# Kernel tuning notes

Hardware: AMD Instinct MI355X
Metric: run time of the kernel (lower is better)

Reference implementation:

```python
import jax, jax.numpy as jnp
import numpy as np

# Module hyperparameters (from init_kwargs)
H, E, K = 16, 8, 2          # heads, experts per head, top-k
P, PV = 64, 64              # q/k and v projection sizes
D = 1024                    # state / input / output size
B, T = 8, 512               # batch, sequence length (self-attention)
R = 2 * T - 1               # number of relative offsets


def setup_inputs() -> dict:
    key = jax.random.key(0)
    ks = jax.random.split(key, 9)
    std_in = 1.0 / np.sqrt(D)
    std_out = 1.0 / np.sqrt(H * PV)
    return {
        "x": jax.random.normal(ks[0], (B, T, D), jnp.float32),
        "pe": jax.random.normal(ks[1], (R, D), jnp.float32),
        "w_sel_o": jax.random.normal(ks[2], (H, E, D), jnp.float32) * std_in,
        "w_sel_v": jax.random.normal(ks[3], (H, E, D), jnp.float32) * std_in,
        "W_q": jax.random.normal(ks[4], (H, E, D, P), jnp.float32) * std_in,
        "W_k": jax.random.normal(ks[5], (H, E, D, P), jnp.float32) * std_in,
        "W_v": jax.random.normal(ks[6], (H, E, D, PV), jnp.float32) * std_in,
        "W_o": jax.random.normal(ks[7], (H, E, PV, D), jnp.float32) * std_out,
        "W_pos": jax.random.normal(ks[8], (H * P, D), jnp.float32) * std_in,
    }


def _gates(x, w_sel):
    # sigmoid selection per head, top-K experts kept with their gate values.
    logits = jnp.einsum('btd,hed->bthe', x, w_sel)
    g = jax.nn.sigmoid(logits)
    vals, idx = jax.lax.top_k(g, K)                      # [B,T,H,K]
    onehot = jax.nn.one_hot(idx, E, dtype=g.dtype)        # [B,T,H,K,E]
    return jnp.einsum('bthk,bthke->bthe', vals, onehot)   # sparse dense gates [B,T,H,E]


def _moe_proj(x, W, gates):
    # x [B,T,D], W [H,E,D,P], gates [B,T,H,E] -> [B,T,H,P]
    out = jnp.zeros(x.shape[:2] + (H, W.shape[-1]), x.dtype)
    for e in range(E):  # fixed small expert loop; avoids [B,T,H,E,P] intermediate
        out = out + gates[..., e, None] * jnp.einsum('btd,hdp->bthp', x, W[:, e])
    return out


def reference(x, pe, w_sel_o, w_sel_v, W_q, W_k, W_v, W_o, W_pos):
    # MoEUT selection sharing: q shares o's selection, k shares v's selection.
    g_qo = _gates(x, w_sel_o)
    g_kv = _gates(x, w_sel_v)

    q = _moe_proj(x, W_q, g_qo)   # [B,T,H,P]
    k = _moe_proj(x, W_k, g_kv)   # [B,T,H,P]
    v = _moe_proj(x, W_v, g_kv)   # [B,T,H,PV]

    scale = 1.0 / np.sqrt(P)
    k_pos = (pe @ W_pos.T).reshape(R, H, P)               # relative-position keys

    s_cont = jnp.einsum('bthp,bshp->bhts', q, k)          # content scores
    s_rel = jnp.einsum('bthp,rhp->bhtr', q, k_pos)        # scores over relative offsets
    t_idx = jnp.arange(T)
    rel = t_idx[None, :] - t_idx[:, None] + (T - 1)       # rel index for (t, s)
    s_pos = s_rel[:, :, t_idx[:, None], rel]              # Transformer-XL shift -> [B,H,T,T]

    scores = (s_cont + s_pos) * scale
    causal = t_idx[None, :] <= t_idx[:, None]
    scores = jnp.where(causal[None, None], scores, jnp.asarray(-1e9, scores.dtype))
    attn = jax.nn.softmax(scores, axis=-1)
    ctx = jnp.einsum('bhts,bshv->bthv', attn, v)          # [B,T,H,PV]

    # MoE output projection with o-selection
    out = jnp.zeros((x.shape[0], x.shape[1], W_o.shape[-1]), x.dtype)
    for e in range(E):
        out = out + jnp.einsum('bthv,hvd->btd', ctx * g_qo[..., e, None], W_o[:, e])
    return out
```

## Files before the change

kernel.cpp:

```cpp
#include <hip/hip_runtime.h>
#include <hip/hip_bf16.h>
#include <math.h>

#define H_ 16
#define E_ 8
#define D_ 1024
#define P_ 64
#define PV_ 64
#define B_ 8
#define T_ 512
#define R_ 1023
#define BT_ 4096
#define CAP_ 1024
#define PROWS_ 192
#define PTILES_ 4

typedef __attribute__((ext_vector_type(8))) unsigned short ushort8;
typedef __attribute__((ext_vector_type(4))) unsigned short ushort4v;
typedef __attribute__((ext_vector_type(8))) short short8;
typedef __attribute__((ext_vector_type(4))) float f32x4;

__device__ inline float bf2f(unsigned short u) {
  union { unsigned int i; float f; } c; c.i = ((unsigned int)u) << 16; return c.f;
}
// ... 62 lines not shown
  }
  __syncthreads();

  int wave = tid >> 6, lane = tid & 63;
  const float4* wt4 = (const float4*)wt + (size_t)ks * 256 * 64 + lane;
  float4 acc[8];
#pragma unroll
  for (int r = 0; r < 8; ++r) acc[r] = (float4){0.f, 0.f, 0.f, 0.f};

  for (int k4b = 0; k4b < 64; ++k4b) {
    float4 wv0 = wt4[(size_t)(k4b * 4 + 0) * 64];
    float4 wv1 = wt4[(size_t)(k4b * 4 + 1) * 64];
    float4 wv2 = wt4[(size_t)(k4b * 4 + 2) * 64];
    float4 wv3 = wt4[(size_t)(k4b * 4 + 3) * 64];
#pragma unroll
    for (int r = 0; r < 8; ++r) {
      float4 xv = ((const float4*)xs[wave * 8 + r])[k4b];
      acc[r].x += xv.x * wv0.x + xv.y * wv1.x + xv.z * wv2.x + xv.w * wv3.x;
      acc[r].y += xv.x * wv0.y + xv.y * wv1.y + xv.z * wv2.y + xv.w * wv3.y;
      acc[r].z += xv.x * wv0.z + xv.y * wv1.z + xv.z * wv2.z + xv.w * wv3.z;
      acc[r].w += xv.x * wv0.w + xv.y * wv1.w + xv.z * wv2.w + xv.w * wv3.w;
    }
  }

#pragma unroll
  for (int r = 0; r < 8; ++r)
    *(float4*)&part[((size_t)(bt0 + wave * 8 + r) * 4 + ks) * 256 + lane * 4] =
        acc[r];
}

__global__ __launch_bounds__(256) void gates_combine(
    const float* __restrict__ part, int* __restrict__ cnt,
    int* __restrict__ lidx, float* __restrict__ lg,
    float* __restrict__ coefs) {
  __shared__ float gv[8][2][H_][E_];
  int tid = threadIdx.x;
  int bt0 = blockIdx.x * 8;

  {
    int set = tid >> 7, he = tid & 127;
    int h = he >> 3, e = he & 7;
#pragma unroll
    for (int r = 0; r < 8; ++r) {
      const float* p = &part[(size_t)(bt0 + r) * 4 * 256 + tid];
      float v = ((p[0] + p[256]) + p[512]) + p[768];
      gv[r][set][h][e] = 1.f / (1.f + expf(-v));
    }
  }
  __syncthreads();

  {
    int r = tid >> 5, st = (tid >> 4) & 1, hh = tid & 15;
    int bt = bt0 + r;
    const float* g = gv[r][st][hh];
    int i1 = 0; float v1 = g[0];
    for (int ee = 1; ee < 8; ee++) if (g[ee] > v1) { v1 = g[ee]; i1 = ee; }
    int i2 = (i1 == 0) ? 1 : 0; float v2 = g[i2];
    for (int ee = 0; ee < 8; ee++) {
      if (ee == i1) continue;
      if (g[ee] > v2) { v2 = g[ee]; i2 = ee; }
    }
    int base1 = ((st * H_ + hh) * E_ + i1) * 2 + 0;
    int p1 = atomicAdd(&cnt[base1], 1);
    lidx[(size_t)base1 * CAP_ + p1] = bt;
    lg[(size_t)base1 * CAP_ + p1] = v1;
    int base2 = ((st * H_ + hh) * E_ + i2) * 2 + 1;
    int p2 = atomicAdd(&cnt[base2], 1);
    lidx[(size_t)base2 * CAP_ + p2] = bt;
    lg[(size_t)base2 * CAP_ + p2] = v2;
    if (st == 0) {
#pragma unroll
      for (int ee = 0; ee < 8; ee++) {
        float c = (ee == i1) ? v1 : ((ee == i2) ? v2 : 0.f);
        coefs[((size_t)bt * H_ + hh) * E_ + ee] = c;
      }
    }
  }
}

__global__ __launch_bounds__(256) void proj_q2_mfma(
    const unsigned short* __restrict__ xb, const float* __restrict__ W,
    const int* __restrict__ cnt, const int* __restrict__ lidx,
    const float* __restrict__ lg, unsigned short* __restrict__ out0,
    unsigned short* __restrict__ out1) {
  int he = blockIdx.x, tile = blockIdx.y;
  int base0 = he * 2 + 0, base1 = he * 2 + 1;
  int n0 = cnt[base0], n1 = cnt[base1];
  int start = tile * PROWS_;
  if (start >= n0 && start >= n1) return;
  int m0 = min(PROWS_, max(0, n0 - start));
  int m1 = min(PROWS_, max(0, n1 - start));

  __shared__ int ridx0[PROWS_], ridx1[PROWS_];
  __shared__ float rgs0[PROWS_], rgs1[PROWS_];
  __shared__ __align__(16) unsigned short As0[PROWS_][72];
  __shared__ __align__(16) unsigned short As1[PROWS_][72];
  __shared__ __align__(16) unsigned short Bs[64][72];
  int tid = threadIdx.x;
  for (int i = tid; i < PROWS_; i += 256) {
    int v0i = 0, v1i = 0; float g0 = 0.f, g1 = 0.f;
    if (i < m0) {
      v0i = lidx[(size_t)base0 * CAP_ + start + i];
      g0 = lg[(size_t)base0 * CAP_ + start + i];
    }
    if (i < m1) {
      v1i = lidx[(size_t)base1 * CAP_ + start + i];
      g1 = lg[(size_t)base1 * CAP_ + start + i];
    }
    ridx0[i] = v0i; rgs0[i] = g0;
    ridx1[i] = v1i; rgs1[i] = g1;
  }
  __syncthreads();

  int wave = tid >> 6, lane = tid & 63;
  int lr = lane & 15, lk = (lane >> 4) << 3;
  f32x4 acc0[3][4] = {}, acc1[3][4] = {};
  const float* Wb = W + (size_t)he * D_ * P_;

  int sr = tid >> 2, sseg = (tid & 3) << 4;
  int c4 = (tid & 15) * 4;
  int drb = tid >> 4;

  for (int d0 = 0; d0 < D_; d0 += 64) {
#pragma unroll
    for (int i = 0; i < 3; ++i) {
      int row = i * 64 + sr;
      const unsigned short* x0 = xb + (size_t)ridx0[row] * D_ + d0 + sseg;
      *(ushort8*)&As0[row][sseg] = *(const ushort8*)x0;
      *(ushort8*)&As0[row][sseg + 8] = *(const ushort8*)(x0 + 8);
      const unsigned short* x1 = xb + (size_t)ridx1[row] * D_ + d0 + sseg;
      *(ushort8*)&As1[row][sseg] = *(const ushort8*)x1;
      *(ushort8*)&As1[row][sseg + 8] = *(const ushort8*)(x1 + 8);
    }
#pragma unroll
    for (int pass = 0; pass < 4; ++pass) {
      int dr = pass * 16 + drb;
      float4 wv = *(const float4*)&Wb[(size_t)(d0 + dr) * P_ + c4];
      Bs[c4 + 0][dr] = f2bf(wv.x);
      Bs[c4 + 1][dr] = f2bf(wv.y);
      Bs[c4 + 2][dr] = f2bf(wv.z);
      Bs[c4 + 3][dr] = f2bf(wv.w);
    }
    __syncthreads();
#pragma unroll
    for (int kk = 0; kk < 2; ++kk) {
      short8 af0[3], af1[3], bfr[4];
#pragma unroll
      for (int mm = 0; mm < 3; ++mm) {
        af0[mm] = *(const short8*)&As0[wave * 48 + mm * 16 + lr][kk * 32 + lk];
        af1[mm] = *(const short8*)&As1[wave * 48 + mm * 16 + lr][kk * 32 + lk];
      }
#pragma unroll
      for (int nn = 0; nn < 4; ++nn)
        bfr[nn] = *(const short8*)&Bs[nn * 16 + lr][kk * 32 + lk];
#pragma unroll
      for (int mm = 0; mm < 3; ++mm)
#pragma unroll
        for (int nn = 0; nn < 4; ++nn) {
          acc0[mm][nn] = __builtin_amdgcn_mfma_f32_16x16x32_bf16(
              af0[mm], bfr[nn], acc0[mm][nn], 0, 0, 0);
          acc1[mm][nn] = __builtin_amdgcn_mfma_f32_16x16x32_bf16(
              af1[mm], bfr[nn], acc1[mm][nn], 0, 0, 0);
        }
    }
    __syncthreads();
  }

  int h = he >> 3;
#pragma unroll
  for (int mm = 0; mm < 3; ++mm) {
#pragma unroll
    for (int r = 0; r < 4; ++r) {
      int row = wave * 48 + mm * 16 + (lane >> 4) * 4 + r;
      if (row < m0) {
        int bt = ridx0[row]; float g = rgs0[row];
        int b = bt >> 9, t = bt & 511;
        unsigned short* orow = out0 + ((size_t)((b * H_ + h) * T_) + t) * P_;
#pragma unroll
        for (int nn = 0; nn < 4; ++nn)
          orow[nn * 16 + lr] = f2bf(g * acc0[mm][nn][r]);
      }
      if (row < m1) {
        int bt = ridx1[row]; float g = rgs1[row];
        int b = bt >> 9, t = bt & 511;
        unsigned short* orow = out1 + ((size_t)((b * H_ + h) * T_) + t) * P_;
#pragma unroll
        for (int nn = 0; nn < 4; ++nn)
          orow[nn * 16 + lr] = f2bf(g * acc1[mm][nn][r]);
      }
    }
  }
}

__global__ __launch_bounds__(256) void proj_kv_mfma(
    const unsigned short* __restrict__ xb, const float* __restrict__ Wk,
    const float* __restrict__ Wv, const int* __restrict__ cnt,
    const int* __restrict__ lidx, const float* __restrict__ lg,
    unsigned short* __restrict__ outk, unsigned short* __restrict__ outv,
    int slot) {
  int he = blockIdx.x, tile = blockIdx.y;
  int base = (128 + he) * 2 + slot;
  int n = cnt[base];
  int start = tile * PROWS_;
  if (start >= n) return;
  int m = min(PROWS_, n - start);

  __shared__ int ridx[PROWS_];
  __shared__ float rgs[PROWS_];
  __shared__ __align__(16) unsigned short As[PROWS_][72];
  __shared__ __align__(16) unsigned short Bk[64][72];
  __shared__ __align__(16) unsigned short Bv[64][72];
  int tid = threadIdx.x;
  for (int i = tid; i < PROWS_; i += 256) {
    int vi = 0; float g = 0.f;
    if (i < m) {
      vi = lidx[(size_t)base * CAP_ + start + i];
      g = lg[(size_t)base * CAP_ + start + i];
    }
    ridx[i] = vi; rgs[i] = g;
  }
  __syncthreads();

  int wave = tid >> 6, lane = tid & 63;
  int lr = lane & 15, lk = (lane >> 4) << 3;
  f32x4 acck[3][4] = {}, accv[3][4] = {};
  const float* Wkb = Wk + (size_t)he * D_ * P_;
  const float* Wvb = Wv + (size_t)he * D_ * P_;

  int sr = tid >> 2, sseg = (tid & 3) << 4;
  int c4 = (tid & 15) * 4;
  int drb = tid >> 4;

  for (int d0 = 0; d0 < D_; d0 += 64) {
#pragma unroll
    for (int i = 0; i < 3; ++i) {
      int row = i * 64 + sr;
      const unsigned short* xrow = xb + (size_t)ridx[row] * D_ + d0 + sseg;
      *(ushort8*)&As[row][sseg] = *(const ushort8*)xrow;
      *(ushort8*)&As[row][sseg + 8] = *(const ushort8*)(xrow + 8);
    }
#pragma unroll
    for (int pass = 0; pass < 4; ++pass) {
      int dr = pass * 16 + drb;
      float4 wv = *(const float4*)&Wkb[(size_t)(d0 + dr) * P_ + c4];
      Bk[c4 + 0][dr] = f2bf(wv.x);
      Bk[c4 + 1][dr] = f2bf(wv.y);
      Bk[c4 + 2][dr] = f2bf(wv.z);
      Bk[c4 + 3][dr] = f2bf(wv.w);
      float4 wv2 = *(const float4*)&Wvb[(size_t)(d0 + dr) * P_ + c4];
      Bv[c4 + 0][dr] = f2bf(wv2.x);
      Bv[c4 + 1][dr] = f2bf(wv2.y);
      Bv[c4 + 2][dr] = f2bf(wv2.z);
      Bv[c4 + 3][dr] = f2bf(wv2.w);
    }
    __syncthreads();
#pragma unroll
    for (int kk = 0; kk < 2; ++kk) {
      short8 af[3], b1[4], b2[4];
#pragma unroll
      for (int mm = 0; mm < 3; ++mm)
        af[mm] = *(const short8*)&As[wave * 48 + mm * 16 + lr][kk * 32 + lk];
#pragma unroll
      for (int nn = 0; nn < 4; ++nn) {
        b1[nn] = *(const short8*)&Bk[nn * 16 + lr][kk * 32 + lk];
        b2[nn] = *(const short8*)&Bv[nn * 16 + lr][kk * 32 + lk];
      }
#pragma unroll
      for (int mm = 0; mm < 3; ++mm)
#pragma unroll
        for (int nn = 0; nn < 4; ++nn) {
          acck[mm][nn] = __builtin_amdgcn_mfma_f32_16x16x32_bf16(
              af[mm], b1[nn], acck[mm][nn], 0, 0, 0);
          accv[mm][nn] = __builtin_amdgcn_mfma_f32_16x16x32_bf16(
              af[mm], b2[nn], accv[mm][nn], 0, 0, 0);
        }
    }
    __syncthreads();
  }

  int h = he >> 3;
#pragma unroll
  for (int mm = 0; mm < 3; ++mm) {
#pragma unroll
    for (int r = 0; r < 4; ++r) {
      int row = wave * 48 + mm * 16 + (lane >> 4) * 4 + r;
      if (row < m) {
        int bt = ridx[row]; float g = rgs[row];
        int b = bt >> 9, t = bt & 511;
        size_t off = ((size_t)((b * H_ + h) * T_) + t) * P_;
        unsigned short* okr = outk + off;
        unsigned short* ovr = outv + off;
        if (slot == 0) {
#pragma unroll
          for (int nn = 0; nn < 4; ++nn) {
            okr[nn * 16 + lr] = f2bf(g * acck[mm][nn][r]);
            ovr[nn * 16 + lr] = f2bf(g * accv[mm][nn][r]);
          }
        } else {
#pragma unroll
          for (int nn = 0; nn < 4; ++nn) {
            int c = nn * 16 + lr;
            okr[c] = f2bf(bf2f(okr[c]) + g * acck[mm][nn][r]);
            ovr[c] = f2bf(bf2f(ovr[c]) + g * accv[mm][nn][r]);
          }
        }
      }
    }
  }
}

__global__ __launch_bounds__(256) void cvt_pos_kernel(
    const float* __restrict__ pe, const float* __restrict__ Wp,
    unsigned short* __restrict__ peb, unsigned short* __restrict__ wpb) {
  int bid = blockIdx.x;
  const float* src;
  unsigned short* dst;
  if (bid < R_) { src = pe + (size_t)bid * D_; dst = peb + (size_t)bid * D_; }
  else { src = Wp + (size_t)(bid - R_) * D_; dst = wpb + (size_t)(bid - R_) * D_; }
  int tid = threadIdx.x;
  float4 w = ((const float4*)src)[tid];
  ushort4v o = {f2bf(w.x), f2bf(w.y), f2bf(w.z), f2bf(w.w)};
  *(ushort4v*)&dst[tid * 4] = o;
}

__global__ __launch_bounds__(256) void kpos_mfma(
    const unsigned short* __restrict__ peb, const unsigned short* __restrict__ wpb,
    unsigned short* __restrict__ kposb) {
  __shared__ __align__(16) unsigned short As[64][72];
  __shared__ __align__(16) unsigned short Bs[64][72];
  int tid = threadIdx.x, mt = blockIdx.x, nt = blockIdx.y;
  int wave = tid >> 6, lane = tid & 63;
  int wr = wave >> 1, wc = wave & 1;
  int lrow = lane & 15, lk = (lane >> 4) << 3;
  f32x4 acc[2][2] = {};
  int sr = tid >> 2, sseg = (tid & 3) << 4;

  for (int d0 = 0; d0 < D_; d0 += 64) {
    {
      const unsigned short* arow = &peb[(size_t)(mt * 64 + sr) * D_ + d0 + sseg];
      *(ushort8*)&As[sr][sseg] = *(const ushort8*)arow;
      *(ushort8*)&As[sr][sseg + 8] = *(const ushort8*)(arow + 8);
      const unsigned short* brow = &wpb[(size_t)(nt * 64 + sr) * D_ + d0 + sseg];
      *(ushort8*)&Bs[sr][sseg] = *(const ushort8*)brow;
      *(ushort8*)&Bs[sr][sseg + 8] = *(const ushort8*)(brow + 8);
    }
    __syncthreads();
#pragma unroll
    for (int kk = 0; kk < 2; ++kk) {
      short8 af[2], bfr[2];
#pragma unroll
      for (int mm = 0; mm < 2; ++mm)
        af[mm] = *(const short8*)&As[wr * 32 + mm * 16 + lrow][kk * 32 + lk];
#pragma unroll
      for (int nn = 0; nn < 2; ++nn)
        bfr[nn] = *(const short8*)&Bs[wc * 32 + nn * 16 + lrow][kk * 32 + lk];
#pragma unroll
      for (int mm = 0; mm < 2; ++mm)
#pragma unroll
        for (int nn = 0; nn < 2; ++nn)
          acc[mm][nn] = __builtin_amdgcn_mfma_f32_16x16x32_bf16(
              af[mm], bfr[nn], acc[mm][nn], 0, 0, 0);
    }
    __syncthreads();
  }

  int orow0 = mt * 64 + wr * 32 + (lane >> 4) * 4;
  int ocol0 = nt * 64 + wc * 32 + lrow;
#pragma unroll
  for (int mm = 0; mm < 2; ++mm)
#pragma unroll
    for (int nn = 0; nn < 2; ++nn)
#pragma unroll
      for (int r = 0; r < 4; ++r)
        kposb[(size_t)(orow0 + mm * 16 + r) * 1024 + ocol0 + nn * 16] =
            f2bf(acc[mm][nn][r]);
}

__global__ __launch_bounds__(256) void attn_mfma(
    const unsigned short* __restrict__ q0, const unsigned short* __restrict__ q1,
    const unsigned short* __restrict__ k, const unsigned short* __restrict__ v,
    const unsigned short* __restrict__ kposb, unsigned short* __restrict__ ctx) {
  int b = blockIdx.x, h = blockIdx.y, qt = blockIdx.z;
  int t0 = qt << 6;
  int tid = threadIdx.x, wave = tid >> 6, lane = tid & 63;
  int lr = lane & 15, lkg = lane >> 4;
  int lk = lkg << 3;

  __shared__ __align__(16) unsigned short Ks[64][72];
  __shared__ __align__(16) unsigned short VTs[64][72];
  __shared__ __align__(16) unsigned short Srl[64][136];

  size_t bh = (size_t)(b * H_ + h);
  const unsigned short* kb = k + bh * T_ * 64;
  const unsigned short* vb = v + bh * T_ * 64;

  short8 qf[2];
  {
    size_t qoff = (bh * T_ + (size_t)(t0 + wave * 16 + lr)) * 64;
    const unsigned short* q0r = q0 + qoff;
    const unsigned short* q1r = q1 + qoff;
#pragma unroll
    for (int kk = 0; kk < 2; ++kk) {
      ushort8 a0 = *(const ushort8*)&q0r[kk * 32 + lk];
      ushort8 a1 = *(const ushort8*)&q1r[kk * 32 + lk];
      short8 o;
#pragma unroll
      for (int j = 0; j < 8; ++j)
        o[j] = (short)f2bf(bf2f(a0[j]) + bf2f(a1[j]));
      qf[kk] = o;
    }
  }

  float m_run[4], l_run[4];
  f32x4 oacc[4];
#pragma unroll
  for (int r = 0; r < 4; ++r) { m_run[r] = -1e30f; l_run[r] = 0.f; }
#pragma unroll
  for (int nn = 0; nn < 4; ++nn) oacc[nn] = (f32x4){0.f, 0.f, 0.f, 0.f};

  int row_local = wave * 16 + lkg * 4;
  int krow_s = tid >> 1, kseg_s = (tid & 1) * 32;
  int t2 = tid & 127;
  int vr0 = (t2 & 15) * 4, vcs = (t2 >> 4) * 8;

  for (int st = 0; st <= qt; ++st) {
    int s0 = st << 6;
    if (tid < 128) {
      const unsigned short* krow = kb + (size_t)(s0 + krow_s) * 64 + kseg_s;
#pragma unroll
      for (int i = 0; i < 4; ++i)
        *(ushort8*)&Ks[krow_s][kseg_s + i * 8] = *(const ushort8*)(krow + i * 8);
    } else {
      ushort8 vr[4];
#pragma unroll
      for (int i = 0; i < 4; ++i)
        vr[i] = *(const ushort8*)&vb[(size_t)(s0 + vr0 + i) * 64 + vcs];
#pragma unroll
      for (int j = 0; j < 8; ++j) {
        ushort4v o = {vr[0][j], vr[1][j], vr[2][j], vr[3][j]};
        *(ushort4v*)&VTs[vcs + j][vr0] = o;
      }
    }
    __syncthreads();

    f32x4 sc[4] = {};
#pragma unroll
    for (int kk = 0; kk < 2; ++kk) {
#pragma unroll
      for (int nn = 0; nn < 4; ++nn) {
        short8 bfk = *(const short8*)&Ks[nn * 16 + lr][kk * 32 + lk];
        sc[nn] = __builtin_amdgcn_mfma_f32_16x16x32_bf16(qf[kk], bfk, sc[nn], 0, 0, 0);
      }
    }
    int r_base = s0 - t0 + 448;
    const unsigned short* kpb = kposb + (size_t)r_base * 1024 + h * 64;
    f32x4 srf[8] = {};
#pragma unroll
    for (int kk = 0; kk < 2; ++kk) {
#pragma unroll
      for (int nn = 0; nn < 8; ++nn) {
        short8 bfp = *(const short8*)&kpb[(size_t)(nn * 16 + lr) * 1024 + kk * 32 + lk];
        srf[nn] = __builtin_amdgcn_mfma_f32_16x16x32_bf16(qf[kk], bfp, srf[nn], 0, 0, 0);
      }
    }
#pragma unroll
    for (int nn = 0; nn < 8; ++nn)
#pragma unroll
      for (int r = 0; r < 4; ++r)
        Srl[row_local + r][nn * 16 + lr] = f2bf(srf[nn][r]);

    float sv[4][4];
#pragma unroll
    for (int nn = 0; nn < 4; ++nn) {
#pragma unroll
      for (int r = 0; r < 4; ++r) {
        int row = row_local + r;
        int scc = nn * 16 + lr;
        int rj = scc - row + 63;
        float spos = bf2f(Srl[row][rj]);
        float sval = (sc[nn][r] + spos) * 0.125f;
        sv[nn][r] = ((s0 + scc) <= (t0 + row)) ? sval : -1e9f;
      }
    }
    float alpha[4];
#pragma unroll
    for (int r = 0; r < 4; ++r) {
      float mx = fmaxf(fmaxf(sv[0][r], sv[1][r]), fmaxf(sv[2][r], sv[3][r]));
      mx = fmaxf(mx, __shfl_xor(mx, 1));
      mx = fmaxf(mx, __shfl_xor(mx, 2));
      mx = fmaxf(mx, __shfl_xor(mx, 4));
      mx = fmaxf(mx, __shfl_xor(mx, 8));
      float mn = fmaxf(m_run[r], mx);
      alpha[r] = __expf(m_run[r] - mn);
      m_run[r] = mn;
    }
    float psum[4] = {0.f, 0.f, 0.f, 0.f};
#pragma unroll
    for (int nn = 0; nn < 4; ++nn) {
#pragma unroll
      for (int r = 0; r < 4; ++r) {
        unsigned short pb = f2bf(__expf(sv[nn][r] - m_run[r]));
        Srl[row_local + r][64 + nn * 16 + lr] = pb;
        psum[r] += bf2f(pb);
      }
    }
#pragma unroll
    for (int r = 0; r < 4; ++r) {
      float s = psum[r];
      s += __shfl_xor(s, 1); s += __shfl_xor(s, 2);
      s += __shfl_xor(s, 4); s += __shfl_xor(s, 8);
      l_run[r] = l_run[r] * alpha[r] + s;
#pragma unroll
      for (int nn = 0; nn < 4; ++nn) oacc[nn][r] *= alpha[r];
    }
#pragma unroll
    for (int kk = 0; kk < 2; ++kk) {
      short8 pa = *(const short8*)&Srl[wave * 16 + lr][64 + kk * 32 + lk];
#pragma unroll
      for (int nn = 0; nn < 4; ++nn) {
// ... 73 lines not shown
#pragma unroll
    for (int i = 0; i < 4; ++i) { ra[i] = a[i]; rb[i] = bp[i]; }
    cf = coefs[grow * 128 + he0];
  }

  for (int hh = 0; hh < 64; ++hh) {
#pragma unroll
    for (int i = 0; i < 4; ++i) {
      ushort8 o;
#pragma unroll
      for (int j = 0; j < 8; ++j) o[j] = f2bf(bf2f(ra[i][j]) * cf);
      *(ushort8*)&As[arow][aseg + i * 8] = o;
      *(ushort8*)&Bs[arow][aseg + i * 8] = rb[i];
    }
    __syncthreads();

    if (hh < 63) {
      int he = he0 + hh + 1;
      int h = he >> 3;
      const ushort8* a = (const ushort8*)&ctxu[(grow * 16 + h) * 64 + aseg];
      const ushort8* bp = (const ushort8*)&brp[(size_t)he * 64];
#pragma unroll
      for (int i = 0; i < 4; ++i) { ra[i] = a[i]; rb[i] = bp[i]; }
      cf = coefs[grow * 128 + he];
    }

    __builtin_amdgcn_s_setprio(1);
#pragma unroll
    for (int kk = 0; kk < 2; ++kk) {
      short8 af[4], bfr[4];
#pragma unroll
      for (int m = 0; m < 4; ++m)
        af[m] = *(const short8*)&As[wr * 64 + m * 16 + lrow][kk * 32 + lk];
#pragma unroll
      for (int n = 0; n < 4; ++n)
        bfr[n] = *(const short8*)&Bs[wc * 64 + n * 16 + lrow][kk * 32 + lk];
#pragma unroll
      for (int m = 0; m < 4; ++m)
#pragma unroll
        for (int n = 0; n < 4; ++n)
          acc[m][n] = __builtin_amdgcn_mfma_f32_16x16x32_bf16(
              af[m], bfr[n], acc[m][n], 0, 0, 0);
    }
    __builtin_amdgcn_s_setprio(0);
    __syncthreads();
  }

  float* outp = zh ? out1 : out0;
  int orow0 = mt * 128 + wr * 64 + (lane >> 4) * 4;
  int ocol0 = nt * 128 + wc * 64 + lrow;
#pragma unroll
  for (int m = 0; m < 4; ++m)
#pragma unroll
    for (int n = 0; n < 4; ++n)
#pragma unroll
      for (int r = 0; r < 4; ++r)
        outp[(size_t)(orow0 + m * 16 + r) * 1024 + ocol0 + n * 16] = acc[m][n][r];
}

__global__ __launch_bounds__(256) void out_add_kernel(
    float* __restrict__ out, const float* __restrict__ out2) {
  int i = blockIdx.x * 256 + threadIdx.x;
  float4 a = ((const float4*)out)[i];
  float4 b = ((const float4*)out2)[i];
  a.x += b.x; a.y += b.y; a.z += b.z; a.w += b.w;
  ((float4*)out)[i] = a;
}

extern "C" void kernel_launch(void* const* d_in, const int* in_sizes, int n_in,
                              void* d_out, int out_size, void* d_ws, size_t ws_size,
                              hipStream_t stream) {
  const float* x   = (const float*)d_in[0];
  const float* pe  = (const float*)d_in[1];
  const float* wso = (const float*)d_in[2];
  const float* wsv = (const float*)d_in[3];
  const float* Wq  = (const float*)d_in[4];
  const float* Wk  = (const float*)d_in[5];
  const float* Wv  = (const float*)d_in[6];
  const float* Wo  = (const float*)d_in[7];
  const float* Wp  = (const float*)d_in[8];
  float* out = (float*)d_out;
  char* ws = (char*)d_ws;

  int*   cnt   = (int*)  (ws + 0);
  float* coefs = (float*)(ws + 4096);
  int*   lidx  = (int*)  (ws + 2101248);
  float* lg    = (float*)(ws + 4198400);
  unsigned short* xb    = (unsigned short*)(ws + 6295552);
  unsigned short* kposb = (unsigned short*)(ws + 14684160);
  unsigned short* q0    = (unsigned short*)(ws + 16781312);
  unsigned short* q1    = (unsigned short*)(ws + 25169920);
  unsigned short* k     = (unsigned short*)(ws + 33558528);
  unsigned short* v     = (unsigned short*)(ws + 41947136);
  float* wt    = (float*)(ws + 50335744);
  float* part = (float*)(ws + 16781312);
  unsigned short* peb = (unsigned short*)(ws + 33558528);
  unsigned short* wpb = (unsigned short*)(ws + 35655680);
  __hip_bfloat16* ctx = (__hip_bfloat16*)(ws + 6295552);
  __hip_bfloat16* Wob = (__hip_bfloat16*)(ws + 16781312);
  float* out2 = (float*)(ws + 33558528);

  hipLaunchKernelGGL(zero_cnt_kernel, dim3(1), dim3(512), 0, stream, cnt);
  hipLaunchKernelGGL(xcvt_kernel, dim3(4096), dim3(256), 0, stream, x, xb);
  hipLaunchKernelGGL(wt_transpose_kernel, dim3(4, 16), dim3(256), 0, stream,
                     wso, wsv, wt);
  hipLaunchKernelGGL(gates_gemm, dim3(128, 4), dim3(256), 0, stream,
                     x, wt, part);
  hipLaunchKernelGGL(gates_combine, dim3(512), dim3(256), 0, stream,
                     part, cnt, lidx, lg, coefs);

  hipLaunchKernelGGL(cvt_pos_kernel, dim3(R_ + 1024), dim3(256), 0, stream,
                     pe, Wp, peb, wpb);
  hipLaunchKernelGGL(kpos_mfma, dim3(9, 16), dim3(256), 0, stream, peb, wpb, kposb);

  hipLaunchKernelGGL(proj_q2_mfma, dim3(128, PTILES_), dim3(256), 0, stream,
                     xb, Wq, cnt, lidx, lg, q0, q1);
  hipLaunchKernelGGL(proj_kv_mfma, dim3(128, PTILES_), dim3(256), 0, stream,
                     xb, Wk, Wv, cnt, lidx, lg, k, v, 0);
  hipLaunchKernelGGL(proj_kv_mfma, dim3(128, PTILES_), dim3(256), 0, stream,
                     xb, Wk, Wv, cnt, lidx, lg, k, v, 1);

  hipLaunchKernelGGL(attn_mfma, dim3(B_, H_, 8), dim3(256), 0, stream,
                     q0, q1, k, v, kposb, (unsigned short*)ctx);

  hipLaunchKernelGGL(wo_transpose_kernel, dim3(128, 16), dim3(256), 0, stream,
                     Wo, (__hip_bfloat16*)Wob);

  hipLaunchKernelGGL(moe_out_gemm, dim3(8, 32, 2), dim3(256), 0, stream,
                     ctx, coefs, Wob, out, out2);
  hipLaunchKernelGGL(out_add_kernel, dim3(4096), dim3(256), 0, stream,
                     out, out2);
}
```

Before: 529.4 us.

## Fuse both KV expert-slot projections into one kernel, sum slots in attention

Adds proj_kv2_mfma, which computes the K and V projections for both top-k slots in one pass. Each block loads and converts the Wk/Wv weight tile once, then reuses it for the two gathered row sets, where the old path launched one kernel per slot and reloaded the weights each time. The slot results go to separate k0/k1/v0/v1 buffers that attention sums while staging K/V tiles, which replaces the old accumulation into a shared k/v buffer. The cost is a larger workspace, extra K/V reads inside attention, and a dispatch on ws_size that falls back to the old path when the workspace is too small.

Result: no change. 534.0 us (+0.9%).

```diff
diff --git a/kernel.cpp b/kernel.cpp
--- a/kernel.cpp
+++ b/kernel.cpp
@@ -278,6 +278,159 @@
   }
 }
 
+__global__ __launch_bounds__(256) void proj_kv2_mfma(
+    const unsigned short* __restrict__ xb, const float* __restrict__ Wk,
+    const float* __restrict__ Wv, const int* __restrict__ cnt,
+    const int* __restrict__ lidx, const float* __restrict__ lg,
+    unsigned short* __restrict__ ok0, unsigned short* __restrict__ ov0,
+    unsigned short* __restrict__ ok1, unsigned short* __restrict__ ov1) {
+  int he = blockIdx.x, tile = blockIdx.y;
+  int base0 = (128 + he) * 2 + 0, base1 = (128 + he) * 2 + 1;
+  int n0 = cnt[base0], n1 = cnt[base1];
+  int start = tile * PROWS_;
+  if (start >= n0 && start >= n1) return;
+  int m0 = min(PROWS_, max(0, n0 - start));
+  int m1 = min(PROWS_, max(0, n1 - start));
+
+  __shared__ int ridx0[PROWS_], ridx1[PROWS_];
+  __shared__ float rgs0[PROWS_], rgs1[PROWS_];
+  __shared__ __align__(16) unsigned short As[PROWS_][72];
+  __shared__ __align__(16) unsigned short Bk[64][72];
+  __shared__ __align__(16) unsigned short Bv[64][72];
+  int tid = threadIdx.x;
+  for (int i = tid; i < PROWS_; i += 256) {
+    int v0i = 0, v1i = 0; float g0 = 0.f, g1 = 0.f;
+    if (i < m0) {
+      v0i = lidx[(size_t)base0 * CAP_ + start + i];
+      g0 = lg[(size_t)base0 * CAP_ + start + i];
+    }
+    if (i < m1) {
+      v1i = lidx[(size_t)base1 * CAP_ + start + i];
+      g1 = lg[(size_t)base1 * CAP_ + start + i];
+    }
+    ridx0[i] = v0i; rgs0[i] = g0;
+    ridx1[i] = v1i; rgs1[i] = g1;
+  }
+  __syncthreads();
+
+  int wave = tid >> 6, lane = tid & 63;
+  int lr = lane & 15, lk = (lane >> 4) << 3;
+  f32x4 acck0[3][4] = {}, accv0[3][4] = {};
+  f32x4 acck1[3][4] = {}, accv1[3][4] = {};
+  const float* Wkb = Wk + (size_t)he * D_ * P_;
+  const float* Wvb = Wv + (size_t)he * D_ * P_;
+
+  int sr = tid >> 2, sseg = (tid & 3) << 4;
+  int c4 = (tid & 15) * 4;
+  int drb = tid >> 4;
+
+  for (int d0 = 0; d0 < D_; d0 += 64) {
+#pragma unroll
+    for (int i = 0; i < 3; ++i) {
+      int row = i * 64 + sr;
+      const unsigned short* x0 = xb + (size_t)ridx0[row] * D_ + d0 + sseg;
+      *(ushort8*)&As[row][sseg] = *(const ushort8*)x0;
+      *(ushort8*)&As[row][sseg + 8] = *(const ushort8*)(x0 + 8);
+    }
+#pragma unroll
+    for (int pass = 0; pass < 4; ++pass) {
+      int dr = pass * 16 + drb;
+      float4 wv = *(const float4*)&Wkb[(size_t)(d0 + dr) * P_ + c4];
+      Bk[c4 + 0][dr] = f2bf(wv.x);
+      Bk[c4 + 1][dr] = f2bf(wv.y);
+      Bk[c4 + 2][dr] = f2bf(wv.z);
+      Bk[c4 + 3][dr] = f2bf(wv.w);
+      float4 wv2 = *(const float4*)&Wvb[(size_t)(d0 + dr) * P_ + c4];
+      Bv[c4 + 0][dr] = f2bf(wv2.x);
+      Bv[c4 + 1][dr] = f2bf(wv2.y);
+      Bv[c4 + 2][dr] = f2bf(wv2.z);
+      Bv[c4 + 3][dr] = f2bf(wv2.w);
+    }
+    __syncthreads();
+#pragma unroll
+    for (int kk = 0; kk < 2; ++kk) {
+      short8 af[3], b1[4], b2[4];
+#pragma unroll
+      for (int mm = 0; mm < 3; ++mm)
+        af[mm] = *(const short8*)&As[wave * 48 + mm * 16 + lr][kk * 32 + lk];
+#pragma unroll
+      for (int nn = 0; nn < 4; ++nn) {
+        b1[nn] = *(const short8*)&Bk[nn * 16 + lr][kk * 32 + lk];
+        b2[nn] = *(const short8*)&Bv[nn * 16 + lr][kk * 32 + lk];
+      }
+#pragma unroll
+      for (int mm = 0; mm < 3; ++mm)
+#pragma unroll
+        for (int nn = 0; nn < 4; ++nn) {
+          acck0[mm][nn] = __builtin_amdgcn_mfma_f32_16x16x32_bf16(
+              af[mm], b1[nn], acck0[mm][nn], 0, 0, 0);
+          accv0[mm][nn] = __builtin_amdgcn_mfma_f32_16x16x32_bf16(
+              af[mm], b2[nn], accv0[mm][nn], 0, 0, 0);
+        }
+    }
+    __syncthreads();
+#pragma unroll
+    for (int i = 0; i < 3; ++i) {
+      int row = i * 64 + sr;
+      const unsigned short* x1 = xb + (size_t)ridx1[row] * D_ + d0 + sseg;
+      *(ushort8*)&As[row][sseg] = *(const ushort8*)x1;
+      *(ushort8*)&As[row][sseg + 8] = *(const ushort8*)(x1 + 8);
+    }
+    __syncthreads();
+#pragma unroll
+    for (int kk = 0; kk < 2; ++kk) {
+      short8 af[3], b1[4], b2[4];
+#pragma unroll
+      for (int mm = 0; mm < 3; ++mm)
+        af[mm] = *(const short8*)&As[wave * 48 + mm * 16 + lr][kk * 32 + lk];
+#pragma unroll
+      for (int nn = 0; nn < 4; ++nn) {
+        b1[nn] = *(const short8*)&Bk[nn * 16 + lr][kk * 32 + lk];
+        b2[nn] = *(const short8*)&Bv[nn * 16 + lr][kk * 32 + lk];
+      }
+#pragma unroll
+      for (int mm = 0; mm < 3; ++mm)
+#pragma unroll
+        for (int nn = 0; nn < 4; ++nn) {
+          acck1[mm][nn] = __builtin_amdgcn_mfma_f32_16x16x32_bf16(
+              af[mm], b1[nn], acck1[mm][nn], 0, 0, 0);
+          accv1[mm][nn] = __builtin_amdgcn_mfma_f32_16x16x32_bf16(
+              af[mm], b2[nn], accv1[mm][nn], 0, 0, 0);
+        }
+    }
+    __syncthreads();
+  }
+
+  int h = he >> 3;
+#pragma unroll
+  for (int mm = 0; mm < 3; ++mm) {
+#pragma unroll
+    for (int r = 0; r < 4; ++r) {
+      int row = wave * 48 + mm * 16 + (lane >> 4) * 4 + r;
+      if (row < m0) {
+        int bt = ridx0[row]; float g = rgs0[row];
+        int b = bt >> 9, t = bt & 511;
+        size_t off = ((size_t)((b * H_ + h) * T_) + t) * P_;
+#pragma unroll
+        for (int nn = 0; nn < 4; ++nn) {
+          ok0[off + nn * 16 + lr] = f2bf(g * acck0[mm][nn][r]);
+          ov0[off + nn * 16 + lr] = f2bf(g * accv0[mm][nn][r]);
+        }
+      }
+      if (row < m1) {
+        int bt = ridx1[row]; float g = rgs1[row];
+        int b = bt >> 9, t = bt & 511;
+        size_t off = ((size_t)((b * H_ + h) * T_) + t) * P_;
+#pragma unroll
+        for (int nn = 0; nn < 4; ++nn) {
+          ok1[off + nn * 16 + lr] = f2bf(g * acck1[mm][nn][r]);
+          ov1[off + nn * 16 + lr] = f2bf(g * accv1[mm][nn][r]);
+        }
+      }
+    }
+  }
+}
+
 __global__ __launch_bounds__(256) void proj_kv_mfma(
     const unsigned short* __restrict__ xb, const float* __restrict__ Wk,
     const float* __restrict__ Wv, const int* __restrict__ cnt,
@@ -464,8 +617,10 @@
 
 __global__ __launch_bounds__(256) void attn_mfma(
     const unsigned short* __restrict__ q0, const unsigned short* __restrict__ q1,
-    const unsigned short* __restrict__ k, const unsigned short* __restrict__ v,
-    const unsigned short* __restrict__ kposb, unsigned short* __restrict__ ctx) {
+    const unsigned short* __restrict__ k0, const unsigned short* __restrict__ k1,
+    const unsigned short* __restrict__ v0, const unsigned short* __restrict__ v1,
+    const unsigned short* __restrict__ kposb, unsigned short* __restrict__ ctx,
+    int dual) {
   int b = blockIdx.x, h = blockIdx.y, qt = blockIdx.z;
   int t0 = qt << 6;
   int tid = threadIdx.x, wave = tid >> 6, lane = tid & 63;
@@ -477,8 +632,10 @@
   __shared__ __align__(16) unsigned short Srl[64][136];
 
   size_t bh = (size_t)(b * H_ + h);
-  const unsigned short* kb = k + bh * T_ * 64;
-  const unsigned short* vb = v + bh * T_ * 64;
+  const unsigned short* kb0 = k0 + bh * T_ * 64;
+  const unsigned short* kb1 = k1 + bh * T_ * 64;
+  const unsigned short* vb0 = v0 + bh * T_ * 64;
+  const unsigned short* vb1 = v1 + bh * T_ * 64;
 
   short8 qf[2];
   {
@@ -512,15 +669,38 @@
   for (int st = 0; st <= qt; ++st) {
     int s0 = st << 6;
     if (tid < 128) {
-      const unsigned short* krow = kb + (size_t)(s0 + krow_s) * 64 + kseg_s;
-#pragma unroll
-      for (int i = 0; i < 4; ++i)
-        *(ushort8*)&Ks[krow_s][kseg_s + i * 8] = *(const ushort8*)(krow + i * 8);
+      size_t koff = (size_t)(s0 + krow_s) * 64 + kseg_s;
+      if (dual) {
+#pragma unroll
+        for (int i = 0; i < 4; ++i) {
+          ushort8 a0 = *(const ushort8*)(kb0 + koff + i * 8);
+          ushort8 a1 = *(const ushort8*)(kb1 + koff + i * 8);
+          ushort8 o;
+#pragma unroll
+          for (int j = 0; j < 8; ++j) o[j] = f2bf(bf2f(a0[j]) + bf2f(a1[j]));
+          *(ushort8*)&Ks[krow_s][kseg_s + i * 8] = o;
+        }
+      } else {
+#pragma unroll
+        for (int i = 0; i < 4; ++i)
+          *(ushort8*)&Ks[krow_s][kseg_s + i * 8] = *(const ushort8*)(kb0 + koff + i * 8);
+      }
     } else {
       ushort8 vr[4];
 #pragma unroll
-      for (int i = 0; i < 4; ++i)
-        vr[i] = *(const ushort8*)&vb[(size_t)(s0 + vr0 + i) * 64 + vcs];
+      for (int i = 0; i < 4; ++i) {
+        size_t voff = (size_t)(s0 + vr0 + i) * 64 + vcs;
+        ushort8 a0 = *(const ushort8*)(vb0 + voff);
+        if (dual) {
+          ushort8 a1 = *(const ushort8*)(vb1 + voff);
+          ushort8 o;
+#pragma unroll
+          for (int j = 0; j < 8; ++j) o[j] = f2bf(bf2f(a0[j]) + bf2f(a1[j]));
+          vr[i] = o;
+        } else {
+          vr[i] = a0;
+        }
+      }
 #pragma unroll
       for (int j = 0; j < 8; ++j) {
         ushort4v o = {vr[0][j], vr[1][j], vr[2][j], vr[3][j]};
@@ -760,52 +940,105 @@
   float* out = (float*)d_out;
   char* ws = (char*)d_ws;
 
-  int*   cnt   = (int*)  (ws + 0);
-  float* coefs = (float*)(ws + 4096);
-  int*   lidx  = (int*)  (ws + 2101248);
-  float* lg    = (float*)(ws + 4198400);
-  unsigned short* xb    = (unsigned short*)(ws + 6295552);
-  unsigned short* kposb = (unsigned short*)(ws + 14684160);
-  unsigned short* q0    = (unsigned short*)(ws + 16781312);
-  unsigned short* q1    = (unsigned short*)(ws + 25169920);
-  unsigned short* k     = (unsigned short*)(ws + 33558528);
-  unsigned short* v     = (unsigned short*)(ws + 41947136);
-  float* wt    = (float*)(ws + 50335744);
-  float* part = (float*)(ws + 16781312);
-  unsigned short* peb = (unsigned short*)(ws + 33558528);
-  unsigned short* wpb = (unsigned short*)(ws + 35655680);
-  __hip_bfloat16* ctx = (__hip_bfloat16*)(ws + 6295552);
-  __hip_bfloat16* Wob = (__hip_bfloat16*)(ws + 16781312);
-  float* out2 = (float*)(ws + 33558528);
-
-  hipLaunchKernelGGL(zero_cnt_kernel, dim3(1), dim3(512), 0, stream, cnt);
-  hipLaunchKernelGGL(xcvt_kernel, dim3(4096), dim3(256), 0, stream, x, xb);
-  hipLaunchKernelGGL(wt_transpose_kernel, dim3(4, 16), dim3(256), 0, stream,
-                     wso, wsv, wt);
-  hipLaunchKernelGGL(gates_gemm, dim3(128, 4), dim3(256), 0, stream,
-                     x, wt, part);
-  hipLaunchKernelGGL(gates_combine, dim3(512), dim3(256), 0, stream,
-                     part, cnt, lidx, lg, coefs);
-
-  hipLaunchKernelGGL(cvt_pos_kernel, dim3(R_ + 1024), dim3(256), 0, stream,
-                     pe, Wp, peb, wpb);
-  hipLaunchKernelGGL(kpos_mfma, dim3(9, 16), dim3(256), 0, stream, peb, wpb, kposb);
-
-  hipLaunchKernelGGL(proj_q2_mfma, dim3(128, PTILES_), dim3(256), 0, stream,
-                     xb, Wq, cnt, lidx, lg, q0, q1);
-  hipLaunchKernelGGL(proj_kv_mfma, dim3(128, PTILES_), dim3(256), 0, stream,
-                     xb, Wk, Wv, cnt, lidx, lg, k, v, 0);
-  hipLaunchKernelGGL(proj_kv_mfma, dim3(128, PTILES_), dim3(256), 0, stream,
-                     xb, Wk, Wv, cnt, lidx, lg, k, v, 1);
-
-  hipLaunchKernelGGL(attn_mfma, dim3(B_, H_, 8), dim3(256), 0, stream,
-                     q0, q1, k, v, kposb, (unsigned short*)ctx);
-
-  hipLaunchKernelGGL(wo_transpose_kernel, dim3(128, 16), dim3(256), 0, stream,
-                     Wo, (__hip_bfloat16*)Wob);
-
-  hipLaunchKernelGGL(moe_out_gemm, dim3(8, 32, 2), dim3(256), 0, stream,
-                     ctx, coefs, Wob, out, out2);
-  hipLaunchKernelGGL(out_add_kernel, dim3(4096), dim3(256), 0, stream,
-                     out, out2);
-}
+  bool fused = ws_size >= 67112960ull;
+
+  if (fused) {
+    int*   cnt   = (int*)  (ws + 0);
+    float* coefs = (float*)(ws + 4096);
+    int*   lidx  = (int*)  (ws + 2101248);
+    float* lg    = (float*)(ws + 4198400);
+    unsigned short* xb    = (unsigned short*)(ws + 6295552);
+    unsigned short* kposb = (unsigned short*)(ws + 14684160);
+    unsigned short* q0    = (unsigned short*)(ws + 16781312);
+    unsigned short* q1    = (unsigned short*)(ws + 25169920);
+    unsigned short* k0    = (unsigned short*)(ws + 33558528);
+    unsigned short* k1    = (unsigned short*)(ws + 41947136);
+    unsigned short* v0    = (unsigned short*)(ws + 50335744);
+    unsigned short* v1    = (unsigned short*)(ws + 58724352);
+    float* part = (float*)(ws + 16781312);
+    float* wt   = (float*)(ws + 33558528);
+    unsigned short* peb = (unsigned short*)(ws + 41947136);
+    unsigned short* wpb = (unsigned short*)(ws + 44044288);
+    __hip_bfloat16* ctx = (__hip_bfloat16*)(ws + 6295552);
+    __hip_bfloat16* Wob = (__hip_bfloat16*)(ws + 16781312);
+    float* out2 = (float*)(ws + 33558528);
+
+    hipLaunchKernelGGL(zero_cnt_kernel, dim3(1), dim3(512), 0, stream, cnt);
+    hipLaunchKernelGGL(xcvt_kernel, dim3(4096), dim3(256), 0, stream, x, xb);
+    hipLaunchKernelGGL(wt_transpose_kernel, dim3(4, 16), dim3(256), 0, stream,
+                       wso, wsv, wt);
+    hipLaunchKernelGGL(gates_gemm, dim3(128, 4), dim3(256), 0, stream,
+                       x, wt, part);
+    hipLaunchKernelGGL(gates_combine, dim3(512), dim3(256), 0, stream,
+                       part, cnt, lidx, lg, coefs);
+
+    hipLaunchKernelGGL(cvt_pos_kernel, dim3(R_ + 1024), dim3(256), 0, stream,
+                       pe, Wp, peb, wpb);
+    hipLaunchKernelGGL(kpos_mfma, dim3(9, 16), dim3(256), 0, stream,
+                       peb, wpb, kposb);
+
+    hipLaunchKernelGGL(proj_q2_mfma, dim3(128, PTILES_), dim3(256), 0, stream,
+                       xb, Wq, cnt, lidx, lg, q0, q1);
+    hipLaunchKernelGGL(proj_kv2_mfma, dim3(128, PTILES_), dim3(256), 0, stream,
+                       xb, Wk, Wv, cnt, lidx, lg, k0, v0, k1, v1);
+
+    hipLaunchKernelGGL(attn_mfma, dim3(B_, H_, 8), dim3(256), 0, stream,
+                       q0, q1, k0, k1, v0, v1, kposb, (unsigned short*)ctx, 1);
+
+    hipLaunchKernelGGL(wo_transpose_kernel, dim3(128, 16), dim3(256), 0, stream,
+                       Wo, Wob);
+    hipLaunchKernelGGL(moe_out_gemm, dim3(8, 32, 2), dim3(256), 0, stream,
+                       ctx, coefs, Wob, out, out2);
+    hipLaunchKernelGGL(out_add_kernel, dim3(4096), dim3(256), 0, stream,
+                       out, out2);
+  } else {
+    int*   cnt   = (int*)  (ws + 0);
+    float* coefs = (float*)(ws + 4096);
+    int*   lidx  = (int*)  (ws + 2101248);
+    float* lg    = (float*)(ws + 4198400);
+    unsigned short* xb    = (unsigned short*)(ws + 6295552);
+    unsigned short* kposb = (unsigned short*)(ws + 14684160);
+    unsigned short* q0    = (unsigned short*)(ws + 16781312);
+    unsigned short* q1    = (unsigned short*)(ws + 25169920);
+    unsigned short* k     = (unsigned short*)(ws + 33558528);
+    unsigned short* v     = (unsigned short*)(ws + 41947136);
+    float* wt    = (float*)(ws + 50335744);
+    float* part = (float*)(ws + 16781312);
+    unsigned short* peb = (unsigned short*)(ws + 33558528);
+    unsigned short* wpb = (unsigned short*)(ws + 35655680);
+    __hip_bfloat16* ctx = (__hip_bfloat16*)(ws + 6295552);
+    __hip_bfloat16* Wob = (__hip_bfloat16*)(ws + 16781312);
+    float* out2 = (float*)(ws + 33558528);
+
+    hipLaunchKernelGGL(zero_cnt_kernel, dim3(1), dim3(512), 0, stream, cnt);
+    hipLaunchKernelGGL(xcvt_kernel, dim3(4096), dim3(256), 0, stream, x, xb);
+    hipLaunchKernelGGL(wt_transpose_kernel, dim3(4, 16), dim3(256), 0, stream,
+                       wso, wsv, wt);
+    hipLaunchKernelGGL(gates_gemm, dim3(128, 4), dim3(256), 0, stream,
+                       x, wt, part);
+    hipLaunchKernelGGL(gates_combine, dim3(512), dim3(256), 0, stream,
+                       part, cnt, lidx, lg, coefs);
+
+    hipLaunchKernelGGL(cvt_pos_kernel, dim3(R_ + 1024), dim3(256), 0, stream,
+                       pe, Wp, peb, wpb);
+    hipLaunchKernelGGL(kpos_mfma, dim3(9, 16), dim3(256), 0, stream,
+                       peb, wpb, kposb);
+
+    hipLaunchKernelGGL(proj_q2_mfma, dim3(128, PTILES_), dim3(256), 0, stream,
+                       xb, Wq, cnt, lidx, lg, q0, q1);
+    hipLaunchKernelGGL(proj_kv_mfma, dim3(128, PTILES_), dim3(256), 0, stream,
+                       xb, Wk, Wv, cnt, lidx, lg, k, v, 0);
+    hipLaunchKernelGGL(proj_kv_mfma, dim3(128, PTILES_), dim3(256), 0, stream,
+                       xb, Wk, Wv, cnt, lidx, lg, k, v, 1);
+
+    hipLaunchKernelGGL(attn_mfma, dim3(B_, H_, 8), dim3(256), 0, stream,
+                       q0, q1, k, k, v, v, kposb, (unsigned short*)ctx, 0);
+
+    hipLaunchKernelGGL(wo_transpose_kernel, dim3(128, 16), dim3(256), 0, stream,
+                       Wo, Wob);
+    hipLaunchKernelGGL(moe_out_gemm, dim3(8, 32, 2), dim3(256), 0, stream,
+                       ctx, coefs, Wob, out, out2);
+    hipLaunchKernelGGL(out_add_kernel, dim3(4096), dim3(256), 0, stream,
+                       out, out2);
+  }
+}
```

## Reuse dual-slot projection kernel for K/V, sum slots in attention load

Applied to the files above, without the earlier changes.

Removes the separate proj_kv kernel and its two sequential slot launches, one of which did a read-modify-write accumulation. K and V are now each projected by the dual-slot proj_q2 kernel into two separate buffers, one per top-k slot. The attention kernel loads both slot buffers and adds them while staging tiles into shared memory. This removes the serialized read-modify-write pass and the dependency between launches. In exchange it doubles K/V memory traffic inside attention and reloads x tiles separately for the K and V projections. The workspace layout is reshuffled to make room for the extra buffers.

New measurement: 515.7 us, median of 4. -2.6%, faster.

```diff
diff --git a/kernel.cpp b/kernel.cpp
--- a/kernel.cpp
+++ b/kernel.cpp
@@ -168,9 +168,9 @@
     const unsigned short* __restrict__ xb, const float* __restrict__ W,
     const int* __restrict__ cnt, const int* __restrict__ lidx,
     const float* __restrict__ lg, unsigned short* __restrict__ out0,
-    unsigned short* __restrict__ out1) {
+    unsigned short* __restrict__ out1, int set) {
   int he = blockIdx.x, tile = blockIdx.y;
-  int base0 = he * 2 + 0, base1 = he * 2 + 1;
+  int base0 = (set * 128 + he) * 2 + 0, base1 = (set * 128 + he) * 2 + 1;
   int n0 = cnt[base0], n1 = cnt[base1];
   int start = tile * PROWS_;
   if (start >= n0 && start >= n1) return;
@@ -273,123 +273,6 @@
 #pragma unroll
         for (int nn = 0; nn < 4; ++nn)
           orow[nn * 16 + lr] = f2bf(g * acc1[mm][nn][r]);
-      }
-    }
-  }
-}
-
-__global__ __launch_bounds__(256) void proj_kv_mfma(
-    const unsigned short* __restrict__ xb, const float* __restrict__ Wk,
-    const float* __restrict__ Wv, const int* __restrict__ cnt,
-    const int* __restrict__ lidx, const float* __restrict__ lg,
-    unsigned short* __restrict__ outk, unsigned short* __restrict__ outv,
-    int slot) {
-  int he = blockIdx.x, tile = blockIdx.y;
-  int base = (128 + he) * 2 + slot;
-  int n = cnt[base];
-  int start = tile * PROWS_;
-  if (start >= n) return;
-  int m = min(PROWS_, n - start);
-
-  __shared__ int ridx[PROWS_];
-  __shared__ float rgs[PROWS_];
-  __shared__ __align__(16) unsigned short As[PROWS_][72];
-  __shared__ __align__(16) unsigned short Bk[64][72];
-  __shared__ __align__(16) unsigned short Bv[64][72];
-  int tid = threadIdx.x;
-  for (int i = tid; i < PROWS_; i += 256) {
-    int vi = 0; float g = 0.f;
-    if (i < m) {
-      vi = lidx[(size_t)base * CAP_ + start + i];
-      g = lg[(size_t)base * CAP_ + start + i];
-    }
-    ridx[i] = vi; rgs[i] = g;
-  }
-  __syncthreads();
-
-  int wave = tid >> 6, lane = tid & 63;
-  int lr = lane & 15, lk = (lane >> 4) << 3;
-  f32x4 acck[3][4] = {}, accv[3][4] = {};
-  const float* Wkb = Wk + (size_t)he * D_ * P_;
-  const float* Wvb = Wv + (size_t)he * D_ * P_;
-
-  int sr = tid >> 2, sseg = (tid & 3) << 4;
-  int c4 = (tid & 15) * 4;
-  int drb = tid >> 4;
-
-  for (int d0 = 0; d0 < D_; d0 += 64) {
-#pragma unroll
-    for (int i = 0; i < 3; ++i) {
-      int row = i * 64 + sr;
-      const unsigned short* xrow = xb + (size_t)ridx[row] * D_ + d0 + sseg;
-      *(ushort8*)&As[row][sseg] = *(const ushort8*)xrow;
-      *(ushort8*)&As[row][sseg + 8] = *(const ushort8*)(xrow + 8);
-    }
-#pragma unroll
-    for (int pass = 0; pass < 4; ++pass) {
-      int dr = pass * 16 + drb;
-      float4 wv = *(const float4*)&Wkb[(size_t)(d0 + dr) * P_ + c4];
-      Bk[c4 + 0][dr] = f2bf(wv.x);
-      Bk[c4 + 1][dr] = f2bf(wv.y);
-      Bk[c4 + 2][dr] = f2bf(wv.z);
-      Bk[c4 + 3][dr] = f2bf(wv.w);
-      float4 wv2 = *(const float4*)&Wvb[(size_t)(d0 + dr) * P_ + c4];
-      Bv[c4 + 0][dr] = f2bf(wv2.x);
-      Bv[c4 + 1][dr] = f2bf(wv2.y);
-      Bv[c4 + 2][dr] = f2bf(wv2.z);
-      Bv[c4 + 3][dr] = f2bf(wv2.w);
-    }
-    __syncthreads();
-#pragma unroll
-    for (int kk = 0; kk < 2; ++kk) {
-      short8 af[3], b1[4], b2[4];
-#pragma unroll
-      for (int mm = 0; mm < 3; ++mm)
-        af[mm] = *(const short8*)&As[wave * 48 + mm * 16 + lr][kk * 32 + lk];
-#pragma unroll
-      for (int nn = 0; nn < 4; ++nn) {
-        b1[nn] = *(const short8*)&Bk[nn * 16 + lr][kk * 32 + lk];
-        b2[nn] = *(const short8*)&Bv[nn * 16 + lr][kk * 32 + lk];
-      }
-#pragma unroll
-      for (int mm = 0; mm < 3; ++mm)
-#pragma unroll
-        for (int nn = 0; nn < 4; ++nn) {
-          acck[mm][nn] = __builtin_amdgcn_mfma_f32_16x16x32_bf16(
-              af[mm], b1[nn], acck[mm][nn], 0, 0, 0);
-          accv[mm][nn] = __builtin_amdgcn_mfma_f32_16x16x32_bf16(
-              af[mm], b2[nn], accv[mm][nn], 0, 0, 0);
-        }
-    }
-    __syncthreads();
-  }
-
-  int h = he >> 3;
-#pragma unroll
-  for (int mm = 0; mm < 3; ++mm) {
-#pragma unroll
-    for (int r = 0; r < 4; ++r) {
-      int row = wave * 48 + mm * 16 + (lane >> 4) * 4 + r;
-      if (row < m) {
-        int bt = ridx[row]; float g = rgs[row];
-        int b = bt >> 9, t = bt & 511;
-        size_t off = ((size_t)((b * H_ + h) * T_) + t) * P_;
-        unsigned short* okr = outk + off;
-        unsigned short* ovr = outv + off;
-        if (slot == 0) {
-#pragma unroll
-          for (int nn = 0; nn < 4; ++nn) {
-            okr[nn * 16 + lr] = f2bf(g * acck[mm][nn][r]);
-            ovr[nn * 16 + lr] = f2bf(g * accv[mm][nn][r]);
-          }
-        } else {
-#pragma unroll
-          for (int nn = 0; nn < 4; ++nn) {
-            int c = nn * 16 + lr;
-            okr[c] = f2bf(bf2f(okr[c]) + g * acck[mm][nn][r]);
-            ovr[c] = f2bf(bf2f(ovr[c]) + g * accv[mm][nn][r]);
-          }
-        }
       }
     }
   }
@@ -464,7 +347,8 @@
 
 __global__ __launch_bounds__(256) void attn_mfma(
     const unsigned short* __restrict__ q0, const unsigned short* __restrict__ q1,
-    const unsigned short* __restrict__ k, const unsigned short* __restrict__ v,
+    const unsigned short* __restrict__ k0, const unsigned short* __restrict__ k1,
+    const unsigned short* __restrict__ v0, const unsigned short* __restrict__ v1,
     const unsigned short* __restrict__ kposb, unsigned short* __restrict__ ctx) {
   int b = blockIdx.x, h = blockIdx.y, qt = blockIdx.z;
   int t0 = qt << 6;
@@ -477,8 +361,10 @@
   __shared__ __align__(16) unsigned short Srl[64][136];
 
   size_t bh = (size_t)(b * H_ + h);
-  const unsigned short* kb = k + bh * T_ * 64;
-  const unsigned short* vb = v + bh * T_ * 64;
+  const unsigned short* kb0 = k0 + bh * T_ * 64;
+  const unsigned short* kb1 = k1 + bh * T_ * 64;
+  const unsigned short* vb0 = v0 + bh * T_ * 64;
+  const unsigned short* vb1 = v1 + bh * T_ * 64;
 
   short8 qf[2];
   {
@@ -512,15 +398,28 @@
   for (int st = 0; st <= qt; ++st) {
     int s0 = st << 6;
     if (tid < 128) {
-      const unsigned short* krow = kb + (size_t)(s0 + krow_s) * 64 + kseg_s;
-#pragma unroll
-      for (int i = 0; i < 4; ++i)
-        *(ushort8*)&Ks[krow_s][kseg_s + i * 8] = *(const ushort8*)(krow + i * 8);
+      size_t koff = (size_t)(s0 + krow_s) * 64 + kseg_s;
+#pragma unroll
+      for (int i = 0; i < 4; ++i) {
+        ushort8 a0 = *(const ushort8*)(kb0 + koff + i * 8);
+        ushort8 a1 = *(const ushort8*)(kb1 + koff + i * 8);
+        ushort8 o;
+#pragma unroll
+        for (int j = 0; j < 8; ++j) o[j] = f2bf(bf2f(a0[j]) + bf2f(a1[j]));
+        *(ushort8*)&Ks[krow_s][kseg_s + i * 8] = o;
+      }
     } else {
       ushort8 vr[4];
 #pragma unroll
-      for (int i = 0; i < 4; ++i)
-        vr[i] = *(const ushort8*)&vb[(size_t)(s0 + vr0 + i) * 64 + vcs];
+      for (int i = 0; i < 4; ++i) {
+        size_t voff = (size_t)(s0 + vr0 + i) * 64 + vcs;
+        ushort8 a0 = *(const ushort8*)(vb0 + voff);
+        ushort8 a1 = *(const ushort8*)(vb1 + voff);
+        ushort8 o;
+#pragma unroll
+        for (int j = 0; j < 8; ++j) o[j] = f2bf(bf2f(a0[j]) + bf2f(a1[j]));
+        vr[i] = o;
+      }
 #pragma unroll
       for (int j = 0; j < 8; ++j) {
         ushort4v o = {vr[0][j], vr[1][j], vr[2][j], vr[3][j]};
@@ -768,12 +667,14 @@
   unsigned short* kposb = (unsigned short*)(ws + 14684160);
   unsigned short* q0    = (unsigned short*)(ws + 16781312);
   unsigned short* q1    = (unsigned short*)(ws + 25169920);
-  unsigned short* k     = (unsigned short*)(ws + 33558528);
-  unsigned short* v     = (unsigned short*)(ws + 41947136);
-  float* wt    = (float*)(ws + 50335744);
+  unsigned short* k0    = (unsigned short*)(ws + 33558528);
+  unsigned short* k1    = (unsigned short*)(ws + 41947136);
+  unsigned short* v0    = (unsigned short*)(ws + 50335744);
+  unsigned short* v1    = (unsigned short*)(ws + 58724352);
   float* part = (float*)(ws + 16781312);
-  unsigned short* peb = (unsigned short*)(ws + 33558528);
-  unsigned short* wpb = (unsigned short*)(ws + 35655680);
+  float* wt   = (float*)(ws + 33558528);
+  unsigned short* peb = (unsigned short*)(ws + 41947136);
+  unsigned short* wpb = (unsigned short*)(ws + 44044288);
   __hip_bfloat16* ctx = (__hip_bfloat16*)(ws + 6295552);
   __hip_bfloat16* Wob = (__hip_bfloat16*)(ws + 16781312);
   float* out2 = (float*)(ws + 33558528);
@@ -789,21 +690,21 @@
 
   hipLaunchKernelGGL(cvt_pos_kernel, dim3(R_ + 1024), dim3(256), 0, stream,
                      pe, Wp, peb, wpb);
-  hipLaunchKernelGGL(kpos_mfma, dim3(9, 16), dim3(256), 0, stream, peb, wpb, kposb);
+  hipLaunchKernelGGL(kpos_mfma, dim3(9, 16), dim3(256), 0, stream,
+                     peb, wpb, kposb);
 
   hipLaunchKernelGGL(proj_q2_mfma, dim3(128, PTILES_), dim3(256), 0, stream,
-                     xb, Wq, cnt, lidx, lg, q0, q1);
-  hipLaunchKernelGGL(proj_kv_mfma, dim3(128, PTILES_), dim3(256), 0, stream,
-                     xb, Wk, Wv, cnt, lidx, lg, k, v, 0);
-  hipLaunchKernelGGL(proj_kv_mfma, dim3(128, PTILES_), dim3(256), 0, stream,
-                     xb, Wk, Wv, cnt, lidx, lg, k, v, 1);
+                     xb, Wq, cnt, lidx, lg, q0, q1, 0);
+  hipLaunchKernelGGL(proj_q2_mfma, dim3(128, PTILES_), dim3(256), 0, stream,
+                     xb, Wk, cnt, lidx, lg, k0, k1, 1);
+  hipLaunchKernelGGL(proj_q2_mfma, dim3(128, PTILES_), dim3(256), 0, stream,
+                     xb, Wv, cnt, lidx, lg, v0, v1, 1);
 
   hipLaunchKernelGGL(attn_mfma, dim3(B_, H_, 8), dim3(256), 0, stream,
-                     q0, q1, k, v, kposb, (unsigned short*)ctx);
+                     q0, q1, k0, k1, v0, v1, kposb, (unsigned short*)ctx);
 
   hipLaunchKernelGGL(wo_transpose_kernel, dim3(128, 16), dim3(256), 0, stream,
-                     Wo, (__hip_bfloat16*)Wob);
-
+                     Wo, Wob);
   hipLaunchKernelGGL(moe_out_gemm, dim3(8, 32, 2), dim3(256), 0, stream,
                      ctx, coefs, Wob, out, out2);
   hipLaunchKernelGGL(out_add_kernel, dim3(4096), dim3(256), 0, stream,
```
